# Performance work log

Measured on AMD Instinct MI355X. Metric: run time of the kernel, lower is better.

Reference implementation:

```python
import jax, jax.numpy as jnp
import numpy as np

B = 8           # hardcoded batchsize in the original forward
EPS = 1e-4      # scn.BatchNormalization default eps


def setup_inputs() -> dict:
    key = jax.random.key(0)
    ks = jax.random.split(key, 8)
    Nq, Nkv = 16384, 32768
    dec_in, enc_in, nf = 64, 64, 128
    nbr = jax.random.randint(ks[2], (Nq, 27), 0, Nq, dtype=jnp.int32)
    # center tap of the 3x3x3 submanifold conv is the point itself
    nbr = nbr.at[:, 13].set(jnp.arange(Nq, dtype=jnp.int32))
    return {
        "x_decoder_feat": jax.random.normal(ks[0], (Nq, dec_in), jnp.float32),
        "x_encoder_feat": jax.random.normal(ks[1], (Nkv, enc_in), jnp.float32),
        "nbr_idx": nbr,
        "W_p1": jax.random.normal(ks[3], (27, dec_in, nf), jnp.float32) * 0.05,
        "W_q": jax.random.normal(ks[4], (nf, nf), jnp.float32) * 0.05,
        "W_k": jax.random.normal(ks[5], (enc_in, nf), jnp.float32) * 0.05,
        "W_v": jax.random.normal(ks[6], (enc_in, nf), jnp.float32) * 0.05,
        "W_trans": jax.random.normal(ks[7], (nf, nf), jnp.float32) * 0.05,
        "gamma": jnp.ones((nf,), jnp.float32),
        "beta": jnp.zeros((nf,), jnp.float32),
    }


def reference(x_decoder_feat, x_encoder_feat, nbr_idx, W_p1, W_q, W_k, W_v,
              W_trans, gamma, beta):
    nf = W_q.shape[1]
    # p1: 3x3x3 submanifold conv = gather 27 neighbors, per-offset matmul, sum
    x_dec = jnp.einsum('nkc,kcf->nf', x_decoder_feat[nbr_idx], W_p1)  # [Nq,nf]
    q = (x_dec @ W_q).reshape(B, -1, nf)            # [B, nq, nf]
    k = (x_encoder_feat @ W_k).reshape(B, -1, nf)   # [B, nkv, nf]
    v = (x_encoder_feat @ W_v).reshape(B, -1, nf)
    # per-batch QK^T softmax V (no 1/sqrt(d) scaling in original)
    attn = jax.nn.softmax(jnp.einsum('bqc,bkc->bqk', q, k), axis=-1)
    x_r = jnp.einsum('bqk,bkc->bqc', attn, v).reshape(-1, nf)  # [Nq,nf]
    # trans_conv (1x1) + batchnorm (batch stats over all points)
    t = x_r @ W_trans
    mean = t.mean(axis=0)
    var = t.var(axis=0)
    bn = (t - mean) * jax.lax.rsqrt(var + EPS) * gamma + beta
    return x_dec + bn
```

## Files before the change

kernel.cpp:

```cpp
#include <hip/hip_runtime.h>
#include <math.h>

#define NQ      16384
#define NKV     32768
#define CIN     64
#define NF      128
#define NOFF    27
#define BATCH   8
#define SQ      2048
#define SKV     4096
#define BN_EPS  1e-4f
#define SPLIT   4
#define KV_PER_SPLIT (SKV / SPLIT)
#define TILES_PER_SPLIT (KV_PER_SPLIT / 64)
#define SOFTMAX_SHIFT 40.0f

typedef unsigned short u16;
typedef __attribute__((ext_vector_type(4))) float f32x4;
typedef __attribute__((ext_vector_type(8))) short s16x8;

__device__ __forceinline__ u16 f2b(float x) {
    union { float f; unsigned u; } c; c.f = x;
    unsigned r = (c.u + 0x7FFFu + ((c.u >> 16) & 1u)) >> 16;
    return (u16)r;
}
__device__ __forceinline__ float b2f(u16 x) {
    union { unsigned u; float f; } c; c.u = ((unsigned)x) << 16;
    return c.f;
}
__device__ __forceinline__ void g2l16(const void* gp, void* lp) {
    __builtin_amdgcn_global_load_lds(
        (const __attribute__((address_space(1))) unsigned*)gp,
        (__attribute__((address_space(3))) unsigned*)lp, 16, 0, 0);
}

__device__ __forceinline__ void wtrans_one(
    const float* __restrict__ src, u16* __restrict__ dst, int K, int id)
{
    int n  = id / (K / 4);
    int k4 = (id % (K / 4)) * 4;
    const float* s = src + (size_t)k4 * NF + n;
    ushort4 o;
    o.x = f2b(s[0]); o.y = f2b(s[NF]); o.z = f2b(s[2 * NF]); o.w = f2b(s[3 * NF]);
    *(ushort4*)(dst + (size_t)n * K + k4) = o;
}

__global__ __launch_bounds__(256) void cvt_all_kernel(
    const float* __restrict__ xdec_feat, const float* __restrict__ xenc_feat,
    const float* __restrict__ Wp1,
    const float* __restrict__ Wq, const float* __restrict__ Wk,
    const float* __restrict__ Wv, const float* __restrict__ Wt,
    u16* __restrict__ xf_bf, u16* __restrict__ xenc_b, u16* __restrict__ wp1t,
    u16* __restrict__ wqT, u16* __restrict__ wkT,
    u16* __restrict__ wvT, u16* __restrict__ wtT)
{
    int bid = blockIdx.x;
    int t   = threadIdx.x;
    if (bid < 1024) {
        int i = (bid * 256 + t) * 4;
        float4 v = *(const float4*)(xdec_feat + i);
        ushort4 o;
        o.x = f2b(v.x); o.y = f2b(v.y); o.z = f2b(v.z); o.w = f2b(v.w);
        *(ushort4*)(xf_bf + i) = o;
    } else if (bid < 3072) {
        int i = ((bid - 1024) * 256 + t) * 4;
        float4 v = *(const float4*)(xenc_feat + i);
        ushort4 o;
        o.x = f2b(v.x); o.y = f2b(v.y); o.z = f2b(v.z); o.w = f2b(v.w);
        *(ushort4*)(xenc_b + i) = o;
    } else if (bid < 3288) {
        int id = (bid - 3072) * 256 + t;
        int ko = id >> 11;
        int r  = id & 2047;
        int f  = r >> 4;
        int c4 = (r & 15) * 4;
        const float* s = Wp1 + (size_t)ko * 8192 + (size_t)c4 * NF + f;
        ushort4 o;
        o.x = f2b(s[0]); o.y = f2b(s[NF]); o.z = f2b(s[2 * NF]); o.w = f2b(s[3 * NF]);
        *(ushort4*)(wp1t + (size_t)ko * 8192 + (size_t)f * 64 + c4) = o;
    } else {
        int id = (bid - 3288) * 256 + t;
        if (id < 4096)        wtrans_one(Wq, wqT, 128, id);
        else if (id < 6144)   wtrans_one(Wk, wkT, 64, id - 4096);
        else if (id < 8192)   wtrans_one(Wv, wvT, 64, id - 6144);
        else                  wtrans_one(Wt, wtT, 128, id - 8192);
    }
}

__global__ __launch_bounds__(256) void p1conv_mfma_kernel(
    const u16* __restrict__ xf, const int* __restrict__ nbr,
    const u16* __restrict__ wt, float* __restrict__ out,
    u16* __restrict__ outb)
{
    __shared__ u16 Bs[64][64];
    __shared__ int nbr_s[64][28];

    const int t    = threadIdx.x;
    const int w    = t >> 6;
    const int lane = t & 63;
    const int quad = lane >> 4;
    const int l15  = lane & 15;
    const int base = blockIdx.x * 64;
    const int fh   = blockIdx.y;

    for (int i = t; i < 64 * NOFF; i += 256)
        nbr_s[i / NOFF][i % NOFF] = nbr[(size_t)base * NOFF + i];
    __syncthreads();

    f32x4 oacc[4];
    #pragma unroll
    for (int n = 0; n < 4; n++) oacc[n] = (f32x4)0.f;

    const int arow = w * 16 + l15;
    const int srow = w * 16 + (lane >> 3);
    const int k8   = (lane & 7) ^ (srow & 7);

    for (int ko = 0; ko < NOFF; ko++) {
        if (ko) __syncthreads();
        #pragma unroll
        for (int c = 0; c < 2; c++) {
            int row = srow + c * 8;
            int kk  = (lane & 7) ^ (row & 7);
            g2l16(wt + (size_t)ko * 8192 + (size_t)(fh * 64 + row) * 64 + kk * 8,
                  &Bs[w * 16 + c * 8][0]);
        }
        int nb = nbr_s[arow][ko];
        const u16* ap = xf + (size_t)nb * CIN + quad * 8;
        s16x8 af0 = *(const s16x8*)(ap);
        s16x8 af1 = *(const s16x8*)(ap + 32);
        __syncthreads();
        #pragma unroll
        for (int nt = 0; nt < 4; nt++) {
            int p0 = quad ^ (l15 & 7);
            int p1 = (4 + quad) ^ (l15 & 7);
            s16x8 bf0 = *(const s16x8*)&Bs[nt * 16 + l15][p0 * 8];
            s16x8 bf1 = *(const s16x8*)&Bs[nt * 16 + l15][p1 * 8];
            oacc[nt] = __builtin_amdgcn_mfma_f32_16x16x32_bf16(af0, bf0, oacc[nt], 0, 0, 0);
            oacc[nt] = __builtin_amdgcn_mfma_f32_16x16x32_bf16(af1, bf1, oacc[nt], 0, 0, 0);
        }
    }
    #pragma unroll
    for (int nt = 0; nt < 4; nt++)
        #pragma unroll
        for (int r = 0; r < 4; r++) {
            size_t idx = (size_t)(base + w * 16 + quad * 4 + r) * NF + fh * 64 + nt * 16 + l15;
            out[idx]  = oacc[nt][r];
            outb[idx] = f2b(oacc[nt][r]);
        }
}

__global__ __launch_bounds__(256) void gemm_q_kernel(
    const u16* __restrict__ A, const u16* __restrict__ WT, u16* __restrict__ C)
{
    const int t    = threadIdx.x;
    const int w    = t >> 6;
    const int lane = t & 63;
    const int quad = lane >> 4;
    const int l15  = lane & 15;
    const int m0   = blockIdx.x * 64 + w * 16;

    s16x8 af[4];
    const u16* Ap = A + (size_t)(m0 + l15) * NF + quad * 8;
    #pragma unroll
    for (int ks = 0; ks < 4; ks++) af[ks] = *(const s16x8*)(Ap + ks * 32);

    #pragma unroll
    for (int nt = 0; nt < 8; nt++) {
        f32x4 acc = (f32x4)0.f;
        const u16* Wp = WT + (size_t)(nt * 16 + l15) * NF + quad * 8;
        #pragma unroll
        for (int ks = 0; ks < 4; ks++) {
            s16x8 bf = *(const s16x8*)(Wp + ks * 32);
            acc = __builtin_amdgcn_mfma_f32_16x16x32_bf16(af[ks], bf, acc, 0, 0, 0);
        }
        #pragma unroll
        for (int r = 0; r < 4; r++)
            C[(size_t)(m0 + quad * 4 + r) * NF + nt * 16 + l15] = f2b(acc[r]);
    }
}

__global__ __launch_bounds__(256) void gemm_kv_kernel(
    const u16* __restrict__ A, const u16* __restrict__ wkT,
    const u16* __restrict__ wvT, u16* __restrict__ kbuf, u16* __restrict__ vt)
{
    const int t    = threadIdx.x;
    const int w    = t >> 6;
    const int lane = t & 63;
    const int quad = lane >> 4;
    const int l15  = lane & 15;
    const int m0   = blockIdx.x * 64 + w * 16;

    s16x8 af[2];
    const u16* Ap = A + (size_t)(m0 + l15) * CIN + quad * 8;
    af[0] = *(const s16x8*)(Ap);
    af[1] = *(const s16x8*)(Ap + 32);

    int m  = m0 + quad * 4;
    int bb = m >> 12;
    int kv = m & 4095;
    #pragma unroll
    for (int nt = 0; nt < 8; nt++) {
        f32x4 ka = (f32x4)0.f, va = (f32x4)0.f;
        const u16* Kp = wkT + (size_t)(nt * 16 + l15) * CIN + quad * 8;
        const u16* Vp = wvT + (size_t)(nt * 16 + l15) * CIN + quad * 8;
        #pragma unroll
        for (int ks = 0; ks < 2; ks++) {
            s16x8 kb = *(const s16x8*)(Kp + ks * 32);
            s16x8 vb = *(const s16x8*)(Vp + ks * 32);
            ka = __builtin_amdgcn_mfma_f32_16x16x32_bf16(af[ks], kb, ka, 0, 0, 0);
            va = __builtin_amdgcn_mfma_f32_16x16x32_bf16(af[ks], vb, va, 0, 0, 0);
        }
        #pragma unroll
        for (int r = 0; r < 4; r++)
            kbuf[(size_t)(m0 + quad * 4 + r) * NF + nt * 16 + l15] = f2b(ka[r]);
        ushort4 pk;
        pk.x = f2b(va[0]); pk.y = f2b(va[1]); pk.z = f2b(va[2]); pk.w = f2b(va[3]);
        *(ushort4*)(vt + (size_t)(bb * NF + nt * 16 + l15) * SKV + kv) = pk;
    }
}

__global__ __launch_bounds__(256, 3) void attn_mfma_kernel(
    const u16* __restrict__ Q, const u16* __restrict__ K,
    const u16* __restrict__ Vt, u16* __restrict__ Opart,
    float* __restrict__ lpart)
{
    __shared__ u16 Ks[64][128];
    __shared__ u16 Vs[128][64];
    __shared__ u16 Ps[4][16][72];

    const int t    = threadIdx.x;
    const int b    = blockIdx.y;
    const int q0   = blockIdx.x * 64;
    const int sp   = blockIdx.z;
    const int w    = t >> 6;
    const int lane = t & 63;
    const int quad = lane >> 4;
    const int l15  = lane & 15;

    const u16* Kb  = K  + (size_t)b * SKV * NF;
    const u16* Vtb = Vt + (size_t)b * NF * SKV;

    const u16* Qp = Q + ((size_t)(b * SQ + q0 + w * 16 + l15)) * NF + quad * 8;
    s16x8 qf[4];
    #pragma unroll
    for (int ks = 0; ks < 4; ks++) qf[ks] = *(const s16x8*)(Qp + ks * 32);

    f32x4 oacc[8];
    #pragma unroll
    for (int n = 0; n < 8; n++) oacc[n] = (f32x4)0.f;
    float lrow = 0.f;

    const int kvbase = sp * KV_PER_SPLIT;

    for (int tile = 0; tile < TILES_PER_SPLIT; tile++) {
        int kv0 = kvbase + tile * 64;
        __syncthreads();
        #pragma unroll
        for (int c = 0; c < 4; c++) {
            int row = w * 16 + c * 4 + (lane >> 4);
            int k8  = (lane & 15) ^ (row & 15);
            g2l16(Kb + (size_t)(kv0 + row) * NF + k8 * 8, &Ks[w * 16 + c * 4][0]);
        }
        #pragma unroll
        for (int c = 0; c < 4; c++) {
            int row = w * 32 + c * 8 + (lane >> 3);
            int k8  = (lane & 7) ^ (row & 7);
            g2l16(Vtb + (size_t)row * SKV + kv0 + k8 * 8, &Vs[w * 32 + c * 8][0]);
        }
        __syncthreads();

        f32x4 sacc[4];
        #pragma unroll
        for (int c = 0; c < 4; c++) {
            sacc[c] = (f32x4)0.f;
            #pragma unroll
            for (int ks = 0; ks < 4; ks++) {
                int p = (ks * 4 + quad) ^ l15;
                s16x8 ka = *(const s16x8*)&Ks[c * 16 + l15][p * 8];
                sacc[c] = __builtin_amdgcn_mfma_f32_16x16x32_bf16(ka, qf[ks], sacc[c], 0, 0, 0);
            }
        }

        float pv[4][4];
        float rs = 0.f;
        #pragma unroll
        for (int c = 0; c < 4; c++)
            #pragma unroll
            for (int r = 0; r < 4; r++) {
                float p = __expf(sacc[c][r] - SOFTMAX_SHIFT);
                pv[c][r] = p;
                rs += p;
            }
        rs += __shfl_xor(rs, 16);
        rs += __shfl_xor(rs, 32);
        lrow += rs;

        #pragma unroll
        for (int c = 0; c < 4; c++) {
            ushort4 pk;
            pk.x = f2b(pv[c][0]); pk.y = f2b(pv[c][1]);
            pk.z = f2b(pv[c][2]); pk.w = f2b(pv[c][3]);
            *(ushort4*)&Ps[w][l15][c * 16 + quad * 4] = pk;
        }

        s16x8 pb0 = *(const s16x8*)&Ps[w][l15][quad * 8];
        s16x8 pb1 = *(const s16x8*)&Ps[w][l15][32 + quad * 8];
        #pragma unroll
        for (int mt = 0; mt < 8; mt++) {
            int p0 = quad ^ (l15 & 7);
            int p1 = (4 + quad) ^ (l15 & 7);
            s16x8 va0 = *(const s16x8*)&Vs[mt * 16 + l15][p0 * 8];
            s16x8 va1 = *(const s16x8*)&Vs[mt * 16 + l15][p1 * 8];
            oacc[mt] = __builtin_amdgcn_mfma_f32_16x16x32_bf16(va0, pb0, oacc[mt], 0, 0, 0);
            oacc[mt] = __builtin_amdgcn_mfma_f32_16x16x32_bf16(va1, pb1, oacc[mt], 0, 0, 0);
        }
    }

    int grow = b * SQ + q0 + w * 16 + l15;
    u16* Ob = Opart + (size_t)sp * NQ * NF + (size_t)grow * NF;
    #pragma unroll
    for (int mt = 0; mt < 8; mt++) {
        ushort4 ov;
        ov.x = f2b(oacc[mt][0]); ov.y = f2b(oacc[mt][1]);
        ov.z = f2b(oacc[mt][2]); ov.w = f2b(oacc[mt][3]);
        *(ushort4*)(Ob + mt * 16 + quad * 4) = ov;
    }
    if (quad == 0) lpart[sp * NQ + grow] = lrow;
}

__global__ __launch_bounds__(256) void tgemm_fused_kernel(
    const u16* __restrict__ Opart, const float* __restrict__ lpart,
    const u16* __restrict__ WT, float* __restrict__ C, float* __restrict__ stats)
{
    const int t    = threadIdx.x;
    const int w    = t >> 6;
    const int lane = t & 63;
    const int quad = lane >> 4;
    const int l15  = lane & 15;
    const int m0   = blockIdx.x * 64 + w * 16;
    const int row  = m0 + l15;

    float L = 0.f;
    #pragma unroll
    for (int s = 0; s < SPLIT; s++) L += lpart[s * NQ + row];
    float invL = 1.f / L;

    s16x8 af[4];
    #pragma unroll
    for (int ks = 0; ks < 4; ks++) {
        float sum[8] = {0.f, 0.f, 0.f, 0.f, 0.f, 0.f, 0.f, 0.f};
        #pragma unroll
        for (int s = 0; s < SPLIT; s++) {
            const u16* p = Opart + (size_t)s * NQ * NF + (size_t)row * NF + ks * 32 + quad * 8;
            ushort4 u0 = *(const ushort4*)p;
            ushort4 u1 = *(const ushort4*)(p + 4);
            sum[0] += b2f(u0.x); sum[1] += b2f(u0.y);
            sum[2] += b2f(u0.z); sum[3] += b2f(u0.w);
            sum[4] += b2f(u1.x); sum[5] += b2f(u1.y);
            sum[6] += b2f(u1.z); sum[7] += b2f(u1.w);
        }
        union { u16 a[8]; s16x8 v; } pk;
        #pragma unroll
        for (int j = 0; j < 8; j++) pk.a[j] = f2b(sum[j] * invL);
        af[ks] = pk.v;
    }

    f32x4 oacc[8];
    #pragma unroll
    for (int nt = 0; nt < 8; nt++) {
        oacc[nt] = (f32x4)0.f;
        const u16* Wp = WT + (size_t)(nt * 16 + l15) * NF + quad * 8;
        #pragma unroll
        for (int ks = 0; ks < 4; ks++) {
            s16x8 bf = *(const s16x8*)(Wp + ks * 32);
            oacc[nt] = __builtin_amdgcn_mfma_f32_16x16x32_bf16(af[ks], bf, oacc[nt], 0, 0, 0);
        }
    }

    float s[8], sq[8];
    #pragma unroll
    for (int nt = 0; nt < 8; nt++) {
        s[nt] = 0.f; sq[nt] = 0.f;
        #pragma unroll
        for (int r = 0; r < 4; r++) {
            float v = oacc[nt][r];
            C[(size_t)(m0 + quad * 4 + r) * NF + nt * 16 + l15] = v;
            s[nt] += v; sq[nt] += v * v;
        }
    }
    #pragma unroll
    for (int nt = 0; nt < 8; nt++) {
        s[nt]  += __shfl_xor(s[nt], 16);  s[nt]  += __shfl_xor(s[nt], 32);
        sq[nt] += __shfl_xor(sq[nt], 16); sq[nt] += __shfl_xor(sq[nt], 32);
    }
    __shared__ float red[2][4][128];
    if (quad == 0) {
        #pragma unroll
        for (int nt = 0; nt < 8; nt++) {
            red[0][w][nt * 16 + l15] = s[nt];
            red[1][w][nt * 16 + l15] = sq[nt];
        }
    }
    __syncthreads();
    if (t < 128) {
        float a = red[0][0][t] + red[0][1][t] + red[0][2][t] + red[0][3][t];
        atomicAdd(&stats[t], a);
    } else if (t < 256) {
        int f = t - 128;
        float a = red[1][0][f] + red[1][1][f] + red[1][2][f] + red[1][3][f];
        atomicAdd(&stats[128 + f], a);
    }
}

__global__ __launch_bounds__(256) void bn_finalize(
    const float* __restrict__ tbuf, const float* __restrict__ xdec,
    const float* __restrict__ stats, const float* __restrict__ gamma,
    const float* __restrict__ beta, float* __restrict__ out)
{
    const int g = blockIdx.x * 256 + threadIdx.x;
    const int e = g * 4;
    const int f = e & (NF - 1);
    const float invN = 1.0f / (float)NQ;
    float4 tv = *(const float4*)(tbuf + e);
    float4 xv = *(const float4*)(xdec + e);
    float o[4], tt[4] = {tv.x, tv.y, tv.z, tv.w}, xx[4] = {xv.x, xv.y, xv.z, xv.w};
    #pragma unroll
    for (int u = 0; u < 4; u++) {
        float sum  = stats[f + u];
        float sumq = stats[128 + f + u];
        float mean = sum * invN;
        float var  = sumq * invN - mean * mean;
        float sc   = rsqrtf(var + BN_EPS) * gamma[f + u];
        o[u] = xx[u] + (tt[u] - mean) * sc + beta[f + u];
    }
    float4 ov = make_float4(o[0], o[1], o[2], o[3]);
    *(float4*)(out + e) = ov;
}

extern "C" void kernel_launch(void* const* d_in, const int* in_sizes, int n_in,
                              void* d_out, int out_size, void* d_ws, size_t ws_size,
                              hipStream_t stream) {
    const float* xdec_feat = (const float*)d_in[0];
    const float* xenc_feat = (const float*)d_in[1];
    const int*   nbr       = (const int*)d_in[2];
    const float* Wp1       = (const float*)d_in[3];
    const float* Wq        = (const float*)d_in[4];
    const float* Wk        = (const float*)d_in[5];
    const float* Wv        = (const float*)d_in[6];
    const float* Wt        = (const float*)d_in[7];
    const float* gamma     = (const float*)d_in[8];
    const float* beta      = (const float*)d_in[9];
    float* out = (float*)d_out;

    char* wsb = (char*)d_ws;
    const size_t MB = 1024 * 1024;
    float* xdec   = (float*)(wsb + 0);
    u16*   qbuf   = (u16*)  (wsb + 8 * MB);
    u16*   kbuf   = (u16*)  (wsb + 12 * MB);
    u16*   vt     = (u16*)  (wsb + 20 * MB);
    u16*   opart  = (u16*)  (wsb + 28 * MB);
    u16*   xf_bf  = (u16*)  (wsb + 28 * MB);
    u16*   xenc_b = (u16*)  (wsb + 30 * MB);
    u16*   xdec_b = (u16*)  (wsb + 34 * MB);
    u16*   wp1t   = (u16*)  (wsb + 44 * MB);
    u16*   wqT    = (u16*)  (wsb + 44 * MB + 512 * 1024);
    u16*   wkT    = (u16*)  (wsb + 44 * MB + 512 * 1024 + 32768);
    u16*   wvT    = (u16*)  (wsb + 44 * MB + 512 * 1024 + 49152);
    u16*   wtT    = (u16*)  (wsb + 44 * MB + 512 * 1024 + 65536);
    float* lpart  = (float*)(wsb + 45 * MB);
    float* stats  = (float*)(wsb + 45 * MB + 512 * 1024);
    float* tbuf   = (float*)(wsb + 8 * MB);

    hipMemsetAsync(stats, 0, 256 * sizeof(float), stream);

    cvt_all_kernel<<<3336, 256, 0, stream>>>(
        xdec_feat, xenc_feat, Wp1, Wq, Wk, Wv, Wt,
        xf_bf, xenc_b, wp1t, wqT, wkT, wvT, wtT);
    p1conv_mfma_kernel<<<dim3(NQ / 64, 2), 256, 0, stream>>>(xf_bf, nbr, wp1t, xdec, xdec_b);
    gemm_q_kernel<<<NQ / 64, 256, 0, stream>>>(xdec_b, wqT, qbuf);
    gemm_kv_kernel<<<NKV / 64, 256, 0, stream>>>(xenc_b, wkT, wvT, kbuf, vt);
    attn_mfma_kernel<<<dim3(SQ / 64, BATCH, SPLIT), 256, 0, stream>>>(
        qbuf, kbuf, vt, opart, lpart);
    tgemm_fused_kernel<<<NQ / 64, 256, 0, stream>>>(opart, lpart, wtT, tbuf, stats);
    bn_finalize<<<(NQ * NF) / 1024, 256, 0, stream>>>(tbuf, xdec, stats, gamma, beta, out);
}
```

Measured before the change: 205.9 us.

## Fuse p1 conv, Q projection and KV projection into one kernel

Merges the conv, Q-GEMM and KV-GEMM launches into one kernel whose first 512 blocks compute K/V directly from fp32 encoder features and whose remaining blocks compute the full 128-wide conv output and then the Q projection from shared memory. This drops the encoder bf16 conversion pass, the bf16 xdec buffer round trip, the stats memset and two launches. The conv blocks now cover all 128 output features, which doubles LDS and accumulator usage per block and halves the conv grid parallelism. Workspace offsets are rearranged to fit.

```diff
diff --git a/kernel.cpp b/kernel.cpp
--- a/kernel.cpp
+++ b/kernel.cpp
@@ -45,14 +45,14 @@
     *(ushort4*)(dst + (size_t)n * K + k4) = o;
 }
 
-__global__ __launch_bounds__(256) void cvt_all_kernel(
-    const float* __restrict__ xdec_feat, const float* __restrict__ xenc_feat,
-    const float* __restrict__ Wp1,
+__global__ __launch_bounds__(256) void prep_kernel(
+    const float* __restrict__ xdec_feat, const float* __restrict__ Wp1,
     const float* __restrict__ Wq, const float* __restrict__ Wk,
     const float* __restrict__ Wv, const float* __restrict__ Wt,
-    u16* __restrict__ xf_bf, u16* __restrict__ xenc_b, u16* __restrict__ wp1t,
+    u16* __restrict__ xf_bf, u16* __restrict__ wp1t,
     u16* __restrict__ wqT, u16* __restrict__ wkT,
-    u16* __restrict__ wvT, u16* __restrict__ wtT)
+    u16* __restrict__ wvT, u16* __restrict__ wtT,
+    float* __restrict__ stats)
 {
     int bid = blockIdx.x;
     int t   = threadIdx.x;
@@ -62,14 +62,8 @@
         ushort4 o;
         o.x = f2b(v.x); o.y = f2b(v.y); o.z = f2b(v.z); o.w = f2b(v.w);
         *(ushort4*)(xf_bf + i) = o;
-    } else if (bid < 3072) {
-        int i = ((bid - 1024) * 256 + t) * 4;
-        float4 v = *(const float4*)(xenc_feat + i);
-        ushort4 o;
-        o.x = f2b(v.x); o.y = f2b(v.y); o.z = f2b(v.z); o.w = f2b(v.w);
-        *(ushort4*)(xenc_b + i) = o;
-    } else if (bid < 3288) {
-        int id = (bid - 3072) * 256 + t;
+    } else if (bid < 1240) {
+        int id = (bid - 1024) * 256 + t;
         int ko = id >> 11;
         int r  = id & 2047;
         int f  = r >> 4;
@@ -78,21 +72,27 @@
         ushort4 o;
         o.x = f2b(s[0]); o.y = f2b(s[NF]); o.z = f2b(s[2 * NF]); o.w = f2b(s[3 * NF]);
         *(ushort4*)(wp1t + (size_t)ko * 8192 + (size_t)f * 64 + c4) = o;
-    } else {
-        int id = (bid - 3288) * 256 + t;
+    } else if (bid < 1288) {
+        int id = (bid - 1240) * 256 + t;
         if (id < 4096)        wtrans_one(Wq, wqT, 128, id);
         else if (id < 6144)   wtrans_one(Wk, wkT, 64, id - 4096);
         else if (id < 8192)   wtrans_one(Wv, wvT, 64, id - 6144);
         else                  wtrans_one(Wt, wtT, 128, id - 8192);
-    }
-}
-
-__global__ __launch_bounds__(256) void p1conv_mfma_kernel(
-    const u16* __restrict__ xf, const int* __restrict__ nbr,
-    const u16* __restrict__ wt, float* __restrict__ out,
-    u16* __restrict__ outb)
-{
-    __shared__ u16 Bs[64][64];
+    } else {
+        stats[t] = 0.f;
+    }
+}
+
+__global__ __launch_bounds__(256) void main_fused_kernel(
+    const float* __restrict__ xenc, const u16* __restrict__ xf,
+    const int* __restrict__ nbr, const u16* __restrict__ wp1t,
+    const u16* __restrict__ wqT, const u16* __restrict__ wkT,
+    const u16* __restrict__ wvT,
+    u16* __restrict__ kbuf, u16* __restrict__ vt,
+    float* __restrict__ xdec, u16* __restrict__ qbuf)
+{
+    __shared__ u16 Bs[128][64];
+    __shared__ u16 xq[64][136];
     __shared__ int nbr_s[64][28];
 
     const int t    = threadIdx.x;
@@ -100,29 +100,66 @@
     const int lane = t & 63;
     const int quad = lane >> 4;
     const int l15  = lane & 15;
-    const int base = blockIdx.x * 64;
-    const int fh   = blockIdx.y;
+
+    if (blockIdx.x < 512) {
+        const int m0 = blockIdx.x * 64 + w * 16;
+        const float* Ap = xenc + (size_t)(m0 + l15) * CIN + quad * 8;
+        float4 a0 = *(const float4*)(Ap);
+        float4 a1 = *(const float4*)(Ap + 4);
+        float4 a2 = *(const float4*)(Ap + 32);
+        float4 a3 = *(const float4*)(Ap + 36);
+        union { u16 a[8]; s16x8 v; } p0, p1;
+        p0.a[0] = f2b(a0.x); p0.a[1] = f2b(a0.y); p0.a[2] = f2b(a0.z); p0.a[3] = f2b(a0.w);
+        p0.a[4] = f2b(a1.x); p0.a[5] = f2b(a1.y); p0.a[6] = f2b(a1.z); p0.a[7] = f2b(a1.w);
+        p1.a[0] = f2b(a2.x); p1.a[1] = f2b(a2.y); p1.a[2] = f2b(a2.z); p1.a[3] = f2b(a2.w);
+        p1.a[4] = f2b(a3.x); p1.a[5] = f2b(a3.y); p1.a[6] = f2b(a3.z); p1.a[7] = f2b(a3.w);
+        s16x8 af0 = p0.v, af1 = p1.v;
+
+        int m  = m0 + quad * 4;
+        int bb = m >> 12;
+        int kv = m & 4095;
+        #pragma unroll
+        for (int nt = 0; nt < 8; nt++) {
+            f32x4 ka = (f32x4)0.f, va = (f32x4)0.f;
+            const u16* Kp = wkT + (size_t)(nt * 16 + l15) * CIN + quad * 8;
+            const u16* Vp = wvT + (size_t)(nt * 16 + l15) * CIN + quad * 8;
+            s16x8 kb0 = *(const s16x8*)(Kp);
+            s16x8 kb1 = *(const s16x8*)(Kp + 32);
+            s16x8 vb0 = *(const s16x8*)(Vp);
+            s16x8 vb1 = *(const s16x8*)(Vp + 32);
+            ka = __builtin_amdgcn_mfma_f32_16x16x32_bf16(af0, kb0, ka, 0, 0, 0);
+            ka = __builtin_amdgcn_mfma_f32_16x16x32_bf16(af1, kb1, ka, 0, 0, 0);
+            va = __builtin_amdgcn_mfma_f32_16x16x32_bf16(af0, vb0, va, 0, 0, 0);
+            va = __builtin_amdgcn_mfma_f32_16x16x32_bf16(af1, vb1, va, 0, 0, 0);
+            #pragma unroll
+            for (int r = 0; r < 4; r++)
+                kbuf[(size_t)(m0 + quad * 4 + r) * NF + nt * 16 + l15] = f2b(ka[r]);
+            ushort4 pk;
+            pk.x = f2b(va[0]); pk.y = f2b(va[1]); pk.z = f2b(va[2]); pk.w = f2b(va[3]);
+            *(ushort4*)(vt + (size_t)(bb * NF + nt * 16 + l15) * SKV + kv) = pk;
+        }
+        return;
+    }
+
+    const int base = (blockIdx.x - 512) * 64;
 
     for (int i = t; i < 64 * NOFF; i += 256)
         nbr_s[i / NOFF][i % NOFF] = nbr[(size_t)base * NOFF + i];
     __syncthreads();
 
-    f32x4 oacc[4];
-    #pragma unroll
-    for (int n = 0; n < 4; n++) oacc[n] = (f32x4)0.f;
+    f32x4 oacc[8];
+    #pragma unroll
+    for (int n = 0; n < 8; n++) oacc[n] = (f32x4)0.f;
 
     const int arow = w * 16 + l15;
-    const int srow = w * 16 + (lane >> 3);
-    const int k8   = (lane & 7) ^ (srow & 7);
-
     for (int ko = 0; ko < NOFF; ko++) {
         if (ko) __syncthreads();
         #pragma unroll
-        for (int c = 0; c < 2; c++) {
-            int row = srow + c * 8;
+        for (int c = 0; c < 4; c++) {
+            int row = w * 32 + c * 8 + (lane >> 3);
             int kk  = (lane & 7) ^ (row & 7);
-            g2l16(wt + (size_t)ko * 8192 + (size_t)(fh * 64 + row) * 64 + kk * 8,
-                  &Bs[w * 16 + c * 8][0]);
+            g2l16(wp1t + (size_t)ko * 8192 + (size_t)row * 64 + kk * 8,
+                  &Bs[w * 32 + c * 8][0]);
         }
         int nb = nbr_s[arow][ko];
         const u16* ap = xf + (size_t)nb * CIN + quad * 8;
@@ -130,92 +167,43 @@
         s16x8 af1 = *(const s16x8*)(ap + 32);
         __syncthreads();
         #pragma unroll
-        for (int nt = 0; nt < 4; nt++) {
-            int p0 = quad ^ (l15 & 7);
-            int p1 = (4 + quad) ^ (l15 & 7);
-            s16x8 bf0 = *(const s16x8*)&Bs[nt * 16 + l15][p0 * 8];
-            s16x8 bf1 = *(const s16x8*)&Bs[nt * 16 + l15][p1 * 8];
+        for (int nt = 0; nt < 8; nt++) {
+            int pc0 = quad ^ (l15 & 7);
+            int pc1 = (4 + quad) ^ (l15 & 7);
+            s16x8 bf0 = *(const s16x8*)&Bs[nt * 16 + l15][pc0 * 8];
+            s16x8 bf1 = *(const s16x8*)&Bs[nt * 16 + l15][pc1 * 8];
             oacc[nt] = __builtin_amdgcn_mfma_f32_16x16x32_bf16(af0, bf0, oacc[nt], 0, 0, 0);
             oacc[nt] = __builtin_amdgcn_mfma_f32_16x16x32_bf16(af1, bf1, oacc[nt], 0, 0, 0);
         }
     }
-    #pragma unroll
-    for (int nt = 0; nt < 4; nt++)
+
+    #pragma unroll
+    for (int nt = 0; nt < 8; nt++)
         #pragma unroll
         for (int r = 0; r < 4; r++) {
-            size_t idx = (size_t)(base + w * 16 + quad * 4 + r) * NF + fh * 64 + nt * 16 + l15;
-            out[idx]  = oacc[nt][r];
-            outb[idx] = f2b(oacc[nt][r]);
-        }
-}
-
-__global__ __launch_bounds__(256) void gemm_q_kernel(
-    const u16* __restrict__ A, const u16* __restrict__ WT, u16* __restrict__ C)
-{
-    const int t    = threadIdx.x;
-    const int w    = t >> 6;
-    const int lane = t & 63;
-    const int quad = lane >> 4;
-    const int l15  = lane & 15;
-    const int m0   = blockIdx.x * 64 + w * 16;
-
-    s16x8 af[4];
-    const u16* Ap = A + (size_t)(m0 + l15) * NF + quad * 8;
-    #pragma unroll
-    for (int ks = 0; ks < 4; ks++) af[ks] = *(const s16x8*)(Ap + ks * 32);
+            int row = w * 16 + quad * 4 + r;
+            int col = nt * 16 + l15;
+            xdec[(size_t)(base + row) * NF + col] = oacc[nt][r];
+            xq[row][col] = f2b(oacc[nt][r]);
+        }
+
+    s16x8 aq[4];
+    #pragma unroll
+    for (int ks = 0; ks < 4; ks++)
+        aq[ks] = *(const s16x8*)&xq[w * 16 + l15][ks * 32 + quad * 8];
 
     #pragma unroll
     for (int nt = 0; nt < 8; nt++) {
         f32x4 acc = (f32x4)0.f;
-        const u16* Wp = WT + (size_t)(nt * 16 + l15) * NF + quad * 8;
+        const u16* Wp = wqT + (size_t)(nt * 16 + l15) * NF + quad * 8;
         #pragma unroll
         for (int ks = 0; ks < 4; ks++) {
             s16x8 bf = *(const s16x8*)(Wp + ks * 32);
-            acc = __builtin_amdgcn_mfma_f32_16x16x32_bf16(af[ks], bf, acc, 0, 0, 0);
+            acc = __builtin_amdgcn_mfma_f32_16x16x32_bf16(aq[ks], bf, acc, 0, 0, 0);
         }
         #pragma unroll
         for (int r = 0; r < 4; r++)
-            C[(size_t)(m0 + quad * 4 + r) * NF + nt * 16 + l15] = f2b(acc[r]);
-    }
-}
-
-__global__ __launch_bounds__(256) void gemm_kv_kernel(
-    const u16* __restrict__ A, const u16* __restrict__ wkT,
-    const u16* __restrict__ wvT, u16* __restrict__ kbuf, u16* __restrict__ vt)
-{
-    const int t    = threadIdx.x;
-    const int w    = t >> 6;
-    const int lane = t & 63;
-    const int quad = lane >> 4;
-    const int l15  = lane & 15;
-    const int m0   = blockIdx.x * 64 + w * 16;
-
-    s16x8 af[2];
-    const u16* Ap = A + (size_t)(m0 + l15) * CIN + quad * 8;
-    af[0] = *(const s16x8*)(Ap);
-    af[1] = *(const s16x8*)(Ap + 32);
-
-    int m  = m0 + quad * 4;
-    int bb = m >> 12;
-    int kv = m & 4095;
-    #pragma unroll
-    for (int nt = 0; nt < 8; nt++) {
-        f32x4 ka = (f32x4)0.f, va = (f32x4)0.f;
-        const u16* Kp = wkT + (size_t)(nt * 16 + l15) * CIN + quad * 8;
-        const u16* Vp = wvT + (size_t)(nt * 16 + l15) * CIN + quad * 8;
-        #pragma unroll
-        for (int ks = 0; ks < 2; ks++) {
-            s16x8 kb = *(const s16x8*)(Kp + ks * 32);
-            s16x8 vb = *(const s16x8*)(Vp + ks * 32);
-            ka = __builtin_amdgcn_mfma_f32_16x16x32_bf16(af[ks], kb, ka, 0, 0, 0);
-            va = __builtin_amdgcn_mfma_f32_16x16x32_bf16(af[ks], vb, va, 0, 0, 0);
-        }
-        #pragma unroll
-        for (int r = 0; r < 4; r++)
-            kbuf[(size_t)(m0 + quad * 4 + r) * NF + nt * 16 + l15] = f2b(ka[r]);
-        ushort4 pk;
-        pk.x = f2b(va[0]); pk.y = f2b(va[1]); pk.z = f2b(va[2]); pk.w = f2b(va[3]);
-        *(ushort4*)(vt + (size_t)(bb * NF + nt * 16 + l15) * SKV + kv) = pk;
+            qbuf[(size_t)(base + w * 16 + quad * 4 + r) * NF + nt * 16 + l15] = f2b(acc[r]);
     }
 }
 
@@ -459,26 +447,22 @@
     u16*   kbuf   = (u16*)  (wsb + 12 * MB);
     u16*   vt     = (u16*)  (wsb + 20 * MB);
     u16*   opart  = (u16*)  (wsb + 28 * MB);
-    u16*   xf_bf  = (u16*)  (wsb + 28 * MB);
-    u16*   xenc_b = (u16*)  (wsb + 30 * MB);
-    u16*   xdec_b = (u16*)  (wsb + 34 * MB);
-    u16*   wp1t   = (u16*)  (wsb + 44 * MB);
-    u16*   wqT    = (u16*)  (wsb + 44 * MB + 512 * 1024);
-    u16*   wkT    = (u16*)  (wsb + 44 * MB + 512 * 1024 + 32768);
-    u16*   wvT    = (u16*)  (wsb + 44 * MB + 512 * 1024 + 49152);
-    u16*   wtT    = (u16*)  (wsb + 44 * MB + 512 * 1024 + 65536);
-    float* lpart  = (float*)(wsb + 45 * MB);
-    float* stats  = (float*)(wsb + 45 * MB + 512 * 1024);
-    float* tbuf   = (float*)(wsb + 8 * MB);
-
-    hipMemsetAsync(stats, 0, 256 * sizeof(float), stream);
-
-    cvt_all_kernel<<<3336, 256, 0, stream>>>(
-        xdec_feat, xenc_feat, Wp1, Wq, Wk, Wv, Wt,
-        xf_bf, xenc_b, wp1t, wqT, wkT, wvT, wtT);
-    p1conv_mfma_kernel<<<dim3(NQ / 64, 2), 256, 0, stream>>>(xf_bf, nbr, wp1t, xdec, xdec_b);
-    gemm_q_kernel<<<NQ / 64, 256, 0, stream>>>(xdec_b, wqT, qbuf);
-    gemm_kv_kernel<<<NKV / 64, 256, 0, stream>>>(xenc_b, wkT, wvT, kbuf, vt);
+    u16*   xf_bf  = (u16*)  (wsb + 44 * MB);
+    u16*   wp1t   = (u16*)  (wsb + 46 * MB);
+    u16*   wqT    = (u16*)  (wsb + 46 * MB + 512 * 1024);
+    u16*   wkT    = (u16*)  (wsb + 46 * MB + 512 * 1024 + 32768);
+    u16*   wvT    = (u16*)  (wsb + 46 * MB + 512 * 1024 + 49152);
+    u16*   wtT    = (u16*)  (wsb + 46 * MB + 512 * 1024 + 65536);
+    float* lpart  = (float*)(wsb + 47 * MB);
+    float* stats  = (float*)(wsb + 47 * MB + 512 * 1024);
+    float* tbuf   = (float*)(wsb + 12 * MB);
+
+    prep_kernel<<<1289, 256, 0, stream>>>(
+        xdec_feat, Wp1, Wq, Wk, Wv, Wt,
+        xf_bf, wp1t, wqT, wkT, wvT, wtT, stats);
+    main_fused_kernel<<<768, 256, 0, stream>>>(
+        xenc_feat, xf_bf, nbr, wp1t, wqT, wkT, wvT,
+        kbuf, vt, xdec, qbuf);
     attn_mfma_kernel<<<dim3(SQ / 64, BATCH, SPLIT), 256, 0, stream>>>(
         qbuf, kbuf, vt, opart, lpart);
     tgemm_fused_kernel<<<NQ / 64, 256, 0, stream>>>(opart, lpart, wtT, tbuf, stats);
```

New measurement: 197.4 us. -4.1%, faster.
